# Optimization experiments

Measured on AMD Instinct MI355X. Metric: run time of the kernel, lower is better.

The kernel has to match this reference:

```python
import jax, jax.numpy as jnp
import numpy as np

B, L, DM = 2, 4096, 1024
DI = 2048      # expand * d_model
DT = 64        # dt_rank = ceil(d_model/16)
K = 4          # d_conv


def _silu(v):
    return v * jax.nn.sigmoid(v)


def setup_inputs() -> dict:
    key = jax.random.key(0)
    ks = jax.random.split(key, 9)
    s = lambda k, shape, sc: jax.random.normal(k, shape, dtype=jnp.float32) * sc
    return {
        "x": s(ks[0], (B, L, DM), 1.0),
        "in_proj_w": s(ks[1], (2 * DI, DM), 0.02),
        "conv_w": s(ks[2], (DI, 1, K), 0.1),   # depthwise: [out=DI, in/groups=1, k]
        "conv_b": s(ks[3], (DI,), 0.02),
        "x_proj_w": s(ks[4], (DT, DI), 0.02),
        "dt_proj_w": s(ks[5], (DI, DT), 0.02),
        "dt_proj_b": s(ks[6], (DI,), 0.02),
        "A_log": jax.random.uniform(ks[7], (DI,), jnp.float32, -3.0, -1.0),
        "D": jnp.ones((DI,), jnp.float32),
        "out_proj_w": s(ks[8], (DM, DI), 0.02),
    }


def reference(x, in_proj_w, conv_w, conv_b, x_proj_w, dt_proj_w, dt_proj_b,
              A_log, D, out_proj_w):
    b, l, _ = x.shape
    # input projection and gate split
    xz = jnp.einsum('bld,ed->ble', x, in_proj_w)          # [b,l,2*DI]
    xi, z = jnp.split(xz, 2, axis=-1)                     # each [b,l,DI]
    # depthwise causal conv1d (torch: padding=K-1 both sides, keep first L)
    xc = jnp.transpose(xi, (0, 2, 1))                     # [b,DI,l]
    xc = jax.lax.conv_general_dilated(
        xc, conv_w, window_strides=(1,), padding=[(K - 1, 0)],
        dimension_numbers=('NCH', 'OIH', 'NCH'),
        feature_group_count=xc.shape[1])
    xc = xc + conv_b[None, :, None]
    xi = _silu(jnp.transpose(xc, (0, 2, 1)))              # [b,l,DI]
    # dt path: x_proj -> dt_rank, dt_proj -> d_inner, softplus + clamp
    dt_low = jnp.einsum('bld,rd->blr', xi, x_proj_w)      # [b,l,DT]
    delta = jax.nn.softplus(jnp.einsum('blr,dr->bld', dt_low, dt_proj_w) + dt_proj_b)
    delta = jnp.clip(delta, 1e-6, 10.0)                   # [b,l,DI]
    A = jnp.clip(-jnp.exp(A_log), -10.0, -1e-6)           # [DI]
    e = jnp.clip(jnp.exp(delta * A), 1e-6, 1.0)           # decay factors [b,l,DI]

    # selective scan: state = clip(state*e + u)
    def step(state, eu):
        et, ut = eu
        state = jnp.clip(state * et + ut, -1e4, 1e4)
        return state, state

    init = jnp.zeros((b, xi.shape[-1]), xi.dtype)
    _, states = jax.lax.scan(step, init,
                             (jnp.swapaxes(e, 0, 1), jnp.swapaxes(xi, 0, 1)))
    y = jnp.swapaxes(states, 0, 1) + xi * D               # skip connection
    y = jnp.clip(y, -1e4, 1e4)
    y = y * _silu(z)                                      # gate
    return jnp.einsum('bld,ed->ble', y, out_proj_w)       # [b,l,DM]
```

## Files before the change

kernel.cpp:

```cpp
#include <hip/hip_runtime.h>
#include <cstdint>
#include <cstddef>

#define B_   2
#define L_   4096
#define DM_  1024
#define DI_  2048
#define DT_  64
#define M_   (B_*L_)
#define G_   64
#define CH_  (L_/G_)
#define KSPL 8
#define KSL  (DI_/KSPL)
#define BK_  32
#define LDC  136
#define LDCF 68
#define LDC3 132

typedef __bf16 bf16;
typedef __bf16 bf16x8 __attribute__((ext_vector_type(8)));
typedef __bf16 bf16x4 __attribute__((ext_vector_type(4)));
typedef float  f32x4  __attribute__((ext_vector_type(4)));

__device__ __forceinline__ float silu_f(float x){ return x / (1.f + __expf(-x)); }
__device__ __forceinline__ float softplus_f(float x){
  return fmaxf(x, 0.f) + __logf(1.f + __expf(-fabsf(x)));
}
__device__ __forceinline__ float e_of(float delta, float Ad){
  float ee = __expf(delta * Ad);
  return fminf(fmaxf(ee, 1e-6f), 1.f);
}
__device__ __forceinline__ float a_of(const float* alog, int d){
  float Ad = -__expf(alog[d]);
  return fminf(fmaxf(Ad, -10.f), -1e-6f);
}

__device__ __forceinline__ void gl_lds16(const bf16* g, bf16* l){
  __builtin_amdgcn_global_load_lds(
      (const __attribute__((address_space(1))) void*)g,
      (__attribute__((address_space(3))) void*)l, 16, 0, 0);
}

__global__ __launch_bounds__(256)
void cvt_all_kernel(const float4* __restrict__ s0, bf16x4* __restrict__ d0, int n0,
                    const float4* __restrict__ s1, bf16x4* __restrict__ d1, int n1,
                    const float4* __restrict__ s2, bf16x4* __restrict__ d2, int n2,
                    const float4* __restrict__ s3, bf16x4* __restrict__ d3, int n3,
                    const float4* __restrict__ s4, bf16x4* __restrict__ d4, int n4)
{
  int i = blockIdx.x*256 + threadIdx.x;
  const float4* s; bf16x4* d;
  if      (i < n0)                 { s = s0; d = d0; }
  else if ((i -= n0) < n1)         { s = s1; d = d1; }
  else if ((i -= n1) < n2)         { s = s2; d = d2; }
  else if ((i -= n2) < n3)         { s = s3; d = d3; }
  else if ((i -= n3) < n4)         { s = s4; d = d4; }
  else return;
  float4 v = s[i];
  bf16x4 o = {(bf16)v.x, (bf16)v.y, (bf16)v.z, (bf16)v.w};
  d[i] = o;
}

template<int MT, int NT, int KT>
__global__ __launch_bounds__(512, 2)
void gemm256(const bf16* __restrict__ A, const bf16* __restrict__ W,
             bf16* __restrict__ ob, bf16* __restrict__ ob2)
{
  __shared__ __align__(16) char smem[131072];
  char* lA = smem;
  char* lB = smem + 65536;

  const int t    = threadIdx.x;
  const int lane = t & 63;
  const int wave = t >> 6;
  const int wm   = wave >> 2;
  const int wn   = wave & 3;
  const int l16  = lane & 15, quad = lane >> 4;

  const int nnt = NT / 256;
  const int nwg = (MT/256) * nnt;
  const int cpx = nwg >> 3;
  int lin = (blockIdx.x & 7) * cpx + (blockIdx.x >> 3);
  const int m0 = (lin / nnt) * 256;
  const int n0 = (lin % nnt) * 256;

  const int r8     = lane >> 3;
  const int lchunk = (lane & 7) ^ r8;
  const bf16* ap[4]; const bf16* bp[4];
  #pragma unroll
  for (int s = 0; s < 4; ++s){
    ap[s] = A + (size_t)(m0 + s*64 + wave*8 + r8) * KT + lchunk*8;
    bp[s] = W + (size_t)(n0 + s*64 + wave*8 + r8) * KT + lchunk*8;
  }

  auto stage = [&](int ub){
    #pragma unroll
    for (int s = 0; s < 4; ++s){
      gl_lds16(ap[s], (bf16*)(lA + ub*32768 + s*8192 + wave*1024));
      ap[s] += 64;
    }
    #pragma unroll
    for (int s = 0; s < 4; ++s){
      gl_lds16(bp[s], (bf16*)(lB + ub*32768 + s*8192 + wave*1024));
      bp[s] += 64;
    }
  };

  f32x4 acc[8][4] = {};
  constexpr int NTILES = KT / 64;

  stage(0);
  for (int tt = 0; tt < NTILES; ++tt){
    const int u = tt & 1;
    if (tt + 1 < NTILES){
      stage(u ^ 1);
      asm volatile("s_waitcnt vmcnt(8)" ::: "memory");
    } else {
      asm volatile("s_waitcnt vmcnt(0)" ::: "memory");
    }
    __builtin_amdgcn_s_barrier();
    __builtin_amdgcn_sched_barrier(0);
    const char* Ab = lA + u*32768;
    const char* Bb = lB + u*32768;

    bf16x8 a0[8], a1[8], b0[4], b1[4];
    #pragma unroll
    for (int mi = 0; mi < 8; ++mi){
      const int row = wm*128 + mi*16 + l16;
      a0[mi] = *(const bf16x8*)(Ab + row*128 + ((quad ^ (l16 & 7)) << 4));
    }
    #pragma unroll
    for (int ni = 0; ni < 4; ++ni){
      const int row = wn*64 + ni*16 + l16;
      b0[ni] = *(const bf16x8*)(Bb + row*128 + ((quad ^ (l16 & 7)) << 4));
    }
    __builtin_amdgcn_sched_barrier(0);
    #pragma unroll
    for (int mi = 0; mi < 8; ++mi){
      const int row = wm*128 + mi*16 + l16;
      a1[mi] = *(const bf16x8*)(Ab + row*128 + (((4|quad) ^ (l16 & 7)) << 4));
    }
    #pragma unroll
    for (int ni = 0; ni < 4; ++ni){
      const int row = wn*64 + ni*16 + l16;
      b1[ni] = *(const bf16x8*)(Bb + row*128 + (((4|quad) ^ (l16 & 7)) << 4));
    }
    asm volatile("s_waitcnt lgkmcnt(12)" ::: "memory");
    __builtin_amdgcn_sched_barrier(0);
    __builtin_amdgcn_s_setprio(1);
    #pragma unroll
    for (int mi = 0; mi < 8; ++mi)
      #pragma unroll
      for (int ni = 0; ni < 4; ++ni)
        acc[mi][ni] = __builtin_amdgcn_mfma_f32_16x16x32_bf16(
            a0[mi], b0[ni], acc[mi][ni], 0, 0, 0);
    __builtin_amdgcn_s_setprio(0);
    asm volatile("s_waitcnt lgkmcnt(0)" ::: "memory");
    __builtin_amdgcn_sched_barrier(0);
    __builtin_amdgcn_s_setprio(1);
    #pragma unroll
    for (int mi = 0; mi < 8; ++mi)
      #pragma unroll
      for (int ni = 0; ni < 4; ++ni)
        acc[mi][ni] = __builtin_amdgcn_mfma_f32_16x16x32_bf16(
            a1[mi], b1[ni], acc[mi][ni], 0, 0, 0);
    __builtin_amdgcn_s_setprio(0);
    __builtin_amdgcn_sched_barrier(0);
    __builtin_amdgcn_s_barrier();
  }

  bf16* Cs = (bf16*)smem;
  const bool isg  = (n0 >= DI_);
  bf16* outp      = isg ? ob2 : ob;
  const int ncol0 = isg ? (n0 - DI_) : n0;
  #pragma unroll
  for (int pass = 0; pass < 2; ++pass){
    if (wm == pass){
      #pragma unroll
      for (int mi = 0; mi < 8; ++mi)
        #pragma unroll
        for (int ni = 0; ni < 4; ++ni)
          #pragma unroll
          for (int r = 0; r < 4; ++r){
            float v = acc[mi][ni][r];
            if (isg) v = silu_f(v);
            Cs[(mi*16 + quad*4 + r)*264 + wn*64 + ni*16 + l16] = (bf16)v;
          }
    }
    __syncthreads();
    #pragma unroll
    for (int it = 0; it < 8; ++it){
      const int row = it*16 + (t >> 5);
      const int c8  = (t & 31) * 8;
      bf16x8 v = *(const bf16x8*)&Cs[row*264 + c8];
      *(bf16x8*)&outp[(size_t)(m0 + pass*128 + row)*DI_ + ncol0 + c8] = v;
    }
    __syncthreads();
  }
}

template<int EPI, int MT, int NT, int KT>
__global__ __launch_bounds__(256)
void gemm_bt(const bf16* __restrict__ A, const bf16* __restrict__ W,
             float* __restrict__ o0, bf16* __restrict__ ob, bf16* __restrict__ ob2,
             const float* __restrict__ bias, const float* __restrict__ alog,
             const bf16* __restrict__ uq, float* __restrict__ Pq,
             float* __restrict__ Fq)
{
  __shared__ char smem[34816];
  bf16* As = (bf16*)smem;
  bf16* Bs = (bf16*)(smem + 128*BK_*2);
  const int t    = threadIdx.x;
  const int lane = t & 63;
  const int wave = t >> 6;
  const int wm   = wave >> 1, wn = wave & 1;
  const int l16  = lane & 15, quad = lane >> 4;

  int m0, n0;
  if (EPI == 4){
    m0 = blockIdx.y * 128; n0 = 0;
  } else {
    const int gx  = NT / 128;
    const int lin = blockIdx.y * gx + blockIdx.x;
    const int grp = lin / (gx * 4);
    const int rem = lin % (gx * 4);
    m0 = (grp * 4 + (rem & 3)) * 128;
    n0 = (rem >> 2) * 128;
  }

  const int srow = (lane >> 2);
  const int scol = (lane & 3) * 8;

  const int KFULL = (EPI == 4) ? (KT * KSPL) : KT;
  const int kbase = (EPI == 4) ? (int)blockIdx.z * KT : 0;

  const int rowA0 = m0 + wave*32 + srow;
  int rB0 = n0 + wave*32 + srow, rB1 = rB0 + 16;
  if (NT < 128){ rB0 = (rB0 >= NT) ? NT-1 : rB0; rB1 = (rB1 >= NT) ? NT-1 : rB1; }
  const bf16* ap0 = A + (size_t)rowA0*KFULL        + kbase + scol;
  const bf16* ap1 = A + (size_t)(rowA0+16)*KFULL   + kbase + scol;
  const bf16* bp0 = W + (size_t)rB0*KFULL          + kbase + scol;
  const bf16* bp1 = W + (size_t)rB1*KFULL          + kbase + scol;
  bf16* lA0 = &As[(wave*32)*BK_];
  bf16* lA1 = &As[(wave*32+16)*BK_];
  bf16* lB0 = &Bs[(wave*32)*BK_];
  bf16* lB1 = &Bs[(wave*32+16)*BK_];

  f32x4 acc[4][4] = {};
  constexpr int kframes = KT / BK_;

  for (int kt = 0; kt < kframes; ++kt){
    gl_lds16(ap0, lA0);  gl_lds16(ap1, lA1);
    gl_lds16(bp0, lB0);  gl_lds16(bp1, lB1);
    ap0 += BK_; ap1 += BK_; bp0 += BK_; bp1 += BK_;
    __syncthreads();
    bf16x8 af[4], bf_[4];
    #pragma unroll
    for (int i = 0; i < 4; ++i){
      af[i]  = *(const bf16x8*)&As[(wm*64 + i*16 + l16)*BK_ + quad*8];
      bf_[i] = *(const bf16x8*)&Bs[(wn*64 + i*16 + l16)*BK_ + quad*8];
    }
    #pragma unroll
    for (int mi = 0; mi < 4; ++mi)
      #pragma unroll
      for (int ni = 0; ni < 4; ++ni)
        acc[mi][ni] = __builtin_amdgcn_mfma_f32_16x16x32_bf16(af[mi], bf_[ni], acc[mi][ni], 0, 0, 0);
    __syncthreads();
  }

  if (EPI == 3){
    float* Cf = (float*)smem;
    #pragma unroll
    for (int pass = 0; pass < 2; ++pass){
      if (wm == pass){
        #pragma unroll
        for (int mi = 0; mi < 4; ++mi)
          #pragma unroll
          for (int ni = 0; ni < 4; ++ni)
            #pragma unroll
            for (int r = 0; r < 4; ++r)
              Cf[(mi*16 + quad*4 + r)*LDC3 + wn*64 + ni*16 + l16] = acc[mi][ni][r];
      }
      __syncthreads();
      #pragma unroll
      for (int it = 0; it < 8; ++it){
        const int row = it*8 + (t >> 5);
        const int c4  = (t & 31) * 4;
        float4 v = *(const float4*)&Cf[row*LDC3 + c4];
        *(float4*)&o0[(size_t)(m0 + pass*64 + row)*NT + n0 + c4] = v;
      }
      __syncthreads();
    }
  } else if (EPI == 4){
    float* Cf = (float*)smem;
    if (wn == 0){
      #pragma unroll
      for (int mi = 0; mi < 4; ++mi)
        #pragma unroll
        for (int ni = 0; ni < 4; ++ni)
          #pragma unroll
          for (int r = 0; r < 4; ++r)
            Cf[(wm*64 + mi*16 + quad*4 + r)*LDCF + ni*16 + l16] = acc[mi][ni][r];
    }
    __syncthreads();
    #pragma unroll
    for (int it = 0; it < 8; ++it){
      const int row = it*16 + (t >> 4);
      const int c4  = (t & 15) * 4;
      float4 v = *(const float4*)&Cf[row*LDCF + c4];
      *(float4*)&o0[((size_t)blockIdx.z*M_ + m0 + row)*DT_ + c4] = v;
    }
  } else {
    bf16* Cs = (bf16*)smem;
    #pragma unroll
    for (int mi = 0; mi < 4; ++mi){
      #pragma unroll
      for (int ni = 0; ni < 4; ++ni){
        const int n = n0 + wn*64 + ni*16 + l16;
        #pragma unroll
        for (int r = 0; r < 4; ++r){
          float v = acc[mi][ni][r];
          v = softplus_f(v + bias[n]);
          v = fminf(fmaxf(v, 1e-6f), 10.f);
          Cs[(wm*64 + mi*16 + quad*4 + r)*LDC + wn*64 + ni*16 + l16] = (bf16)v;
        }
      }
    }
    __syncthreads();
    #pragma unroll
    for (int it = 0; it < 8; ++it){
      const int row = it*16 + (t >> 4);
      const int c8  = (t & 15) * 8;
      bf16x8 v = *(const bf16x8*)&Cs[row*LDC + c8];
      *(bf16x8*)&ob[(size_t)(m0+row)*NT + n0 + c8] = v;
    }
    {
      const int chunk = t >> 7;
      const int dcol  = t & 127;
      const int dglob = n0 + dcol;
      const float Ad  = a_of(alog, dglob);
      const int b  = m0 >> 12;
      const int c0 = (m0 & 4095) >> 6;
      const size_t ubase = (size_t)(m0 + chunk*64)*DI_ + dglob;
      float p = 1.f, f = 0.f;
      for (int i = 0; i < CH_; ++i){
        float dl = (float)Cs[(chunk*64 + i)*LDC + dcol];
        float ee = e_of(dl, Ad);
        float uu = (float)uq[ubase + (size_t)i*DI_];
        f = f*ee + uu;
        p *= ee;
      }
      const size_t o = ((size_t)(b*G_ + c0 + chunk))*DI_ + dglob;
      Pq[o] = p; Fq[o] = f;
    }
  }
}

__global__ __launch_bounds__(256)
void dt_reduce_kernel(const float* __restrict__ part, bf16* __restrict__ dtl){
  const int i = blockIdx.x*256 + threadIdx.x;
  float s = 0.f;
  #pragma unroll
  for (int z = 0; z < KSPL; ++z) s += part[(size_t)z*M_*DT_ + i];
  dtl[i] = (bf16)s;
}

__global__ __launch_bounds__(256)
void conv_silu_kernel(const bf16* __restrict__ xi, const float* __restrict__ cw,
                      const float* __restrict__ cb, bf16* __restrict__ ubf)
{
  const int idx = blockIdx.x*256 + threadIdx.x;
  const int d = idx & (DI_-1);
  const int l = (idx >> 11) & (L_-1);
  float s = cb[d];
  #pragma unroll
  for (int k = 0; k < 4; ++k){
    const int ll = l + k - 3;
    if (ll >= 0) s += (float)xi[idx + (k-3)*DI_] * cw[d*4 + k];
  }
  ubf[idx] = (bf16)silu_f(s);
}

__global__ __launch_bounds__(256)
void scan_pass3(const bf16* __restrict__ delta, const bf16* __restrict__ u,
                const bf16* __restrict__ g, const float* __restrict__ P,
                const float* __restrict__ F, const float* __restrict__ alog,
                const float* __restrict__ Dp, bf16* __restrict__ y)
{
  const int d = blockIdx.x*256 + threadIdx.x;
  const int c = blockIdx.y, b = blockIdx.z;
  const float Ad = a_of(alog, d);
  float s = 0.f;
  for (int cc = 0; cc < c; ++cc){
    const size_t o = ((size_t)(b*G_ + cc))*DI_ + d;
    s = F[o] + P[o]*s;
  }
  size_t base = ((size_t)(b*L_ + c*CH_))*DI_ + d;
  const float Dd = Dp[d];
  for (int i = 0; i < CH_; ++i){
    const size_t idx = base + (size_t)i*DI_;
    const float uu = (float)u[idx];
    s = s*e_of((float)delta[idx], Ad) + uu;
    float yy = s + uu*Dd;
    yy = fminf(fmaxf(yy, -1e4f), 1e4f);
    yy *= (float)g[idx];
    y[idx] = (bf16)yy;
  }
}

extern "C" void kernel_launch(void* const* d_in, const int* in_sizes, int n_in,
                              void* d_out, int out_size, void* d_ws, size_t ws_size,
                              hipStream_t stream)
{
  (void)in_sizes; (void)n_in; (void)out_size; (void)ws_size;
  const float* x        = (const float*)d_in[0];
  const float* in_w     = (const float*)d_in[1];
  const float* conv_w   = (const float*)d_in[2];
  const float* conv_b   = (const float*)d_in[3];
  const float* xproj_w  = (const float*)d_in[4];
  const float* dtproj_w = (const float*)d_in[5];
  const float* dtproj_b = (const float*)d_in[6];
  const float* A_log    = (const float*)d_in[7];
  const float* Dp       = (const float*)d_in[8];
  const float* out_w    = (const float*)d_in[9];

  char* base = (char*)d_ws;
  const size_t MiB = 1024*1024;
  bf16*  xi_bf = (bf16*) (base + 0);
  float* part  = (float*)(base + 0);
  bf16*  dl_bf = (bf16*) (base + 0);
  bf16*  x_bf  = (bf16*) (base + 32*MiB);
  bf16*  w1_bf = (bf16*) (base + 48*MiB);
  bf16*  g_bf  = (bf16*) (base + 64*MiB);
  bf16*  u_bf  = (bf16*) (base + 96*MiB);
  bf16*  y_bf  = (bf16*) (base + 128*MiB);
  bf16*  wo_bf = (bf16*) (base + 160*MiB);
  bf16*  xp_bf = (bf16*) (base + 164*MiB);
  bf16*  dp_bf = (bf16*) (base + 165*MiB);
  bf16*  dtl_bf= (bf16*) (base + 166*MiB);
  float* P     = (float*)(base + 167*MiB);
  float* F     = (float*)(base + 168*MiB);

  const int c0 = (M_*DM_)/4, c1 = (2*DI_*DM_)/4, c2 = (DT_*DI_)/4,
            c3 = (DI_*DT_)/4, c4 = (DM_*DI_)/4;
  const int ctot = c0+c1+c2+c3+c4;
  cvt_all_kernel<<<(ctot+255)/256, 256, 0, stream>>>(
      (const float4*)x,        (bf16x4*)x_bf,  c0,
      (const float4*)in_w,     (bf16x4*)w1_bf, c1,
      (const float4*)xproj_w,  (bf16x4*)xp_bf, c2,
      (const float4*)dtproj_w, (bf16x4*)dp_bf, c3,
      (const float4*)out_w,    (bf16x4*)wo_bf, c4);

  gemm256<M_, 2*DI_, DM_><<<dim3((M_/256)*((2*DI_)/256)), 512, 0, stream>>>(
      x_bf, w1_bf, xi_bf, g_bf);
  conv_silu_kernel<<<(M_*DI_)/256, 256, 0, stream>>>(xi_bf, conv_w, conv_b, u_bf);
  gemm_bt<4, M_, DT_, KSL><<<dim3(1, M_/128, KSPL), 256, 0, stream>>>(
      u_bf, xp_bf, part, nullptr, nullptr, nullptr,
      nullptr, nullptr, nullptr, nullptr);
  dt_reduce_kernel<<<(M_*DT_)/256, 256, 0, stream>>>(part, dtl_bf);
  gemm_bt<2, M_, DI_, DT_><<<dim3(DI_/128, M_/128), 256, 0, stream>>>(
      dtl_bf, dp_bf, nullptr, dl_bf, nullptr, dtproj_b,
      A_log, u_bf, P, F);
  scan_pass3<<<dim3(DI_/256, G_, B_), 256, 0, stream>>>(
      dl_bf, u_bf, g_bf, P, F, A_log, Dp, y_bf);
  gemm_bt<3, M_, DM_, DI_><<<dim3(DM_/128, M_/128), 256, 0, stream>>>(
      y_bf, wo_bf, (float*)d_out, nullptr, nullptr, nullptr,
      nullptr, nullptr, nullptr, nullptr);
}
```

Before: 399.1 us.

## Route out_proj GEMM through 256x256 pipelined kernel and use inline-asm LDS reads

The output projection GEMM (8192x1024x2048) moves from the simple 128x128 gemm_bt kernel to the double-buffered 256x256 gemm256 kernel. A new fp32 epilogue for gemm256 writes the result in four passes. The LDS fragment loads in gemm256 are also rewritten as inline-asm ds_read_b128 with precomputed swizzled addresses, to cut address arithmetic. The larger tile gives more reuse and better MFMA pipelining, but the grid shrinks to 128 workgroups, which may underfill the GPU.

```diff
diff --git a/kernel.cpp b/kernel.cpp
--- a/kernel.cpp
+++ b/kernel.cpp
@@ -41,6 +41,10 @@
       (__attribute__((address_space(3))) void*)l, 16, 0, 0);
 }
 
+__device__ __forceinline__ void ds_read128(bf16x8& d, uint32_t addr){
+  asm volatile("ds_read_b128 %0, %1" : "=v"(d) : "v"(addr));
+}
+
 __global__ __launch_bounds__(256)
 void cvt_all_kernel(const float4* __restrict__ s0, bf16x4* __restrict__ d0, int n0,
                     const float4* __restrict__ s1, bf16x4* __restrict__ d1, int n1,
@@ -61,10 +65,11 @@
   d[i] = o;
 }
 
-template<int MT, int NT, int KT>
+template<int OUT, int MT, int NT, int KT>
 __global__ __launch_bounds__(512, 2)
 void gemm256(const bf16* __restrict__ A, const bf16* __restrict__ W,
-             bf16* __restrict__ ob, bf16* __restrict__ ob2)
+             bf16* __restrict__ ob, bf16* __restrict__ ob2,
+             float* __restrict__ of)
 {
   __shared__ __align__(16) char smem[131072];
   char* lA = smem;
@@ -105,6 +110,15 @@
       bp[s] += 64;
     }
   };
+
+  const uint32_t lAu = (uint32_t)(uintptr_t)(__attribute__((address_space(3))) char*)lA;
+  const uint32_t lBu = (uint32_t)(uintptr_t)(__attribute__((address_space(3))) char*)lB;
+  const uint32_t swz0 = (uint32_t)(((quad    ) ^ (l16 & 7)) << 4);
+  const uint32_t swz1 = (uint32_t)(((4 | quad) ^ (l16 & 7)) << 4);
+  const uint32_t aB0 = lAu + (uint32_t)((wm*128 + l16) * 128) + swz0;
+  const uint32_t aB1 = lAu + (uint32_t)((wm*128 + l16) * 128) + swz1;
+  const uint32_t bB0 = lBu + (uint32_t)((wn*64  + l16) * 128) + swz0;
+  const uint32_t bB1 = lBu + (uint32_t)((wn*64  + l16) * 128) + swz1;
 
   f32x4 acc[8][4] = {};
   constexpr int NTILES = KT / 64;
@@ -120,31 +134,18 @@
     }
     __builtin_amdgcn_s_barrier();
     __builtin_amdgcn_sched_barrier(0);
-    const char* Ab = lA + u*32768;
-    const char* Bb = lB + u*32768;
+    const uint32_t ub = (uint32_t)(u << 15);
 
     bf16x8 a0[8], a1[8], b0[4], b1[4];
     #pragma unroll
-    for (int mi = 0; mi < 8; ++mi){
-      const int row = wm*128 + mi*16 + l16;
-      a0[mi] = *(const bf16x8*)(Ab + row*128 + ((quad ^ (l16 & 7)) << 4));
-    }
-    #pragma unroll
-    for (int ni = 0; ni < 4; ++ni){
-      const int row = wn*64 + ni*16 + l16;
-      b0[ni] = *(const bf16x8*)(Bb + row*128 + ((quad ^ (l16 & 7)) << 4));
-    }
-    __builtin_amdgcn_sched_barrier(0);
-    #pragma unroll
-    for (int mi = 0; mi < 8; ++mi){
-      const int row = wm*128 + mi*16 + l16;
-      a1[mi] = *(const bf16x8*)(Ab + row*128 + (((4|quad) ^ (l16 & 7)) << 4));
-    }
-    #pragma unroll
-    for (int ni = 0; ni < 4; ++ni){
-      const int row = wn*64 + ni*16 + l16;
-      b1[ni] = *(const bf16x8*)(Bb + row*128 + (((4|quad) ^ (l16 & 7)) << 4));
-    }
+    for (int mi = 0; mi < 8; ++mi) ds_read128(a0[mi], aB0 + ub + mi*2048);
+    #pragma unroll
+    for (int ni = 0; ni < 4; ++ni) ds_read128(b0[ni], bB0 + ub + ni*2048);
+    #pragma unroll
+    for (int mi = 0; mi < 8; ++mi) ds_read128(a1[mi], aB1 + ub + mi*2048);
+    #pragma unroll
+    for (int ni = 0; ni < 4; ++ni) ds_read128(b1[ni], bB1 + ub + ni*2048);
+
     asm volatile("s_waitcnt lgkmcnt(12)" ::: "memory");
     __builtin_amdgcn_sched_barrier(0);
     __builtin_amdgcn_s_setprio(1);
@@ -169,33 +170,60 @@
     __builtin_amdgcn_s_barrier();
   }
 
-  bf16* Cs = (bf16*)smem;
-  const bool isg  = (n0 >= DI_);
-  bf16* outp      = isg ? ob2 : ob;
-  const int ncol0 = isg ? (n0 - DI_) : n0;
-  #pragma unroll
-  for (int pass = 0; pass < 2; ++pass){
-    if (wm == pass){
-      #pragma unroll
-      for (int mi = 0; mi < 8; ++mi)
+  if (OUT == 3){
+    float* Cf = (float*)smem;
+    #pragma unroll
+    for (int pass = 0; pass < 4; ++pass){
+      if (wm == (pass >> 1)){
         #pragma unroll
-        for (int ni = 0; ni < 4; ++ni)
+        for (int mi2 = 0; mi2 < 4; ++mi2){
+          const int mi = (pass & 1)*4 + mi2;
           #pragma unroll
-          for (int r = 0; r < 4; ++r){
-            float v = acc[mi][ni][r];
-            if (isg) v = silu_f(v);
-            Cs[(mi*16 + quad*4 + r)*264 + wn*64 + ni*16 + l16] = (bf16)v;
-          }
-    }
-    __syncthreads();
-    #pragma unroll
-    for (int it = 0; it < 8; ++it){
-      const int row = it*16 + (t >> 5);
-      const int c8  = (t & 31) * 8;
-      bf16x8 v = *(const bf16x8*)&Cs[row*264 + c8];
-      *(bf16x8*)&outp[(size_t)(m0 + pass*128 + row)*DI_ + ncol0 + c8] = v;
-    }
-    __syncthreads();
+          for (int ni = 0; ni < 4; ++ni)
+            #pragma unroll
+            for (int r = 0; r < 4; ++r)
+              Cf[(mi2*16 + quad*4 + r)*264 + wn*64 + ni*16 + l16] = acc[mi][ni][r];
+        }
+      }
+      __syncthreads();
+      #pragma unroll
+      for (int it = 0; it < 8; ++it){
+        const int row = it*8 + (t >> 6);
+        const int c4  = (t & 63) * 4;
+        float4 v = *(const float4*)&Cf[row*264 + c4];
+        *(float4*)&of[(size_t)(m0 + pass*64 + row)*NT + n0 + c4] = v;
+      }
+      __syncthreads();
+    }
+  } else {
+    bf16* Cs = (bf16*)smem;
+    const bool isg  = (n0 >= DI_);
+    bf16* outp      = isg ? ob2 : ob;
+    const int ncol0 = isg ? (n0 - DI_) : n0;
+    #pragma unroll
+    for (int pass = 0; pass < 2; ++pass){
+      if (wm == pass){
+        #pragma unroll
+        for (int mi = 0; mi < 8; ++mi)
+          #pragma unroll
+          for (int ni = 0; ni < 4; ++ni)
+            #pragma unroll
+            for (int r = 0; r < 4; ++r){
+              float v = acc[mi][ni][r];
+              if (isg) v = silu_f(v);
+              Cs[(mi*16 + quad*4 + r)*264 + wn*64 + ni*16 + l16] = (bf16)v;
+            }
+      }
+      __syncthreads();
+      #pragma unroll
+      for (int it = 0; it < 8; ++it){
+        const int row = it*16 + (t >> 5);
+        const int c8  = (t & 31) * 8;
+        bf16x8 v = *(const bf16x8*)&Cs[row*264 + c8];
+        *(bf16x8*)&outp[(size_t)(m0 + pass*128 + row)*DI_ + ncol0 + c8] = v;
+      }
+      __syncthreads();
+    }
   }
 }
 
@@ -268,30 +296,7 @@
     __syncthreads();
   }
 
-  if (EPI == 3){
-    float* Cf = (float*)smem;
-    #pragma unroll
-    for (int pass = 0; pass < 2; ++pass){
-      if (wm == pass){
-        #pragma unroll
-        for (int mi = 0; mi < 4; ++mi)
-          #pragma unroll
-          for (int ni = 0; ni < 4; ++ni)
-            #pragma unroll
-            for (int r = 0; r < 4; ++r)
-              Cf[(mi*16 + quad*4 + r)*LDC3 + wn*64 + ni*16 + l16] = acc[mi][ni][r];
-      }
-      __syncthreads();
-      #pragma unroll
-      for (int it = 0; it < 8; ++it){
-        const int row = it*8 + (t >> 5);
-        const int c4  = (t & 31) * 4;
-        float4 v = *(const float4*)&Cf[row*LDC3 + c4];
-        *(float4*)&o0[(size_t)(m0 + pass*64 + row)*NT + n0 + c4] = v;
-      }
-      __syncthreads();
-    }
-  } else if (EPI == 4){
+  if (EPI == 4){
     float* Cf = (float*)smem;
     if (wn == 0){
       #pragma unroll
@@ -451,8 +456,8 @@
       (const float4*)dtproj_w, (bf16x4*)dp_bf, c3,
       (const float4*)out_w,    (bf16x4*)wo_bf, c4);
 
-  gemm256<M_, 2*DI_, DM_><<<dim3((M_/256)*((2*DI_)/256)), 512, 0, stream>>>(
-      x_bf, w1_bf, xi_bf, g_bf);
+  gemm256<0, M_, 2*DI_, DM_><<<dim3((M_/256)*((2*DI_)/256)), 512, 0, stream>>>(
+      x_bf, w1_bf, xi_bf, g_bf, nullptr);
   conv_silu_kernel<<<(M_*DI_)/256, 256, 0, stream>>>(xi_bf, conv_w, conv_b, u_bf);
   gemm_bt<4, M_, DT_, KSL><<<dim3(1, M_/128, KSPL), 256, 0, stream>>>(
       u_bf, xp_bf, part, nullptr, nullptr, nullptr,
@@ -463,7 +468,6 @@
       A_log, u_bf, P, F);
   scan_pass3<<<dim3(DI_/256, G_, B_), 256, 0, stream>>>(
       dl_bf, u_bf, g_bf, P, F, A_log, Dp, y_bf);
-  gemm_bt<3, M_, DM_, DI_><<<dim3(DM_/128, M_/128), 256, 0, stream>>>(
-      y_bf, wo_bf, (float*)d_out, nullptr, nullptr, nullptr,
-      nullptr, nullptr, nullptr, nullptr);
-}
+  gemm256<3, M_, DM_, DI_><<<dim3((M_/256)*(DM_/256)), 512, 0, stream>>>(
+      y_bf, wo_bf, nullptr, nullptr, (float*)d_out);
+}
```

Measured after the change: 413.3 us. 1.04x slower.
